# Kernel tuning notes

Hardware: AMD Instinct MI355X
Metric: run time of the kernel (lower is better)

Reference implementation:

```python
import jax, jax.numpy as jnp
import numpy as np

B, S, D = 4, 4096, 1024
THETA = 10000.0


def rope(x):
    # x: [..., S, D]; rotates interleaved (even, odd) dim pairs, standard RoPE.
    s, d = x.shape[-2], x.shape[-1]
    pos = jnp.arange(s, dtype=jnp.float32)
    inv_freq = THETA ** (-jnp.arange(0, d, 2, dtype=jnp.float32) / d)  # [d/2]
    ang = pos[:, None] * inv_freq  # [S, d/2]
    c, sn = jnp.cos(ang), jnp.sin(ang)
    e, o = x[..., ::2], x[..., 1::2]
    re = e * c - o * sn
    ro = e * sn + o * c
    return jnp.stack([re, ro], axis=-1).reshape(x.shape)


def setup_inputs() -> dict:
    key = jax.random.key(0)
    k1, k2, k3, k4 = jax.random.split(key, 4)
    scale = 1.0 / np.sqrt(D)
    return {
        "x": jax.random.normal(k1, (B, S, D), dtype=jnp.float32),
        "Wq": jax.random.normal(k2, (D, D), dtype=jnp.float32) * scale,
        "Wk": jax.random.normal(k3, (D, D), dtype=jnp.float32) * scale,
        "Wv": jax.random.normal(k4, (D, D), dtype=jnp.float32) * scale,
    }


def reference(x, Wq, Wk, Wv):
    # QKV projections (Linear with weight [out, in], no bias)
    Q = rope(x @ Wq.T)
    K = rope(x @ Wk.T)
    V = x @ Wv.T
    d = x.shape[-1]
    s = x.shape[-2]
    scores = jnp.einsum('bqd,bkd->bqk', Q, K) / jnp.sqrt(jnp.asarray(d, Q.dtype))
    causal = jnp.tril(jnp.ones((s, s), dtype=bool))
    scores = jnp.where(causal, scores, -jnp.inf)
    attn = jax.nn.softmax(scores, axis=-1)
    return jnp.einsum('bqk,bkd->bqd', attn, V)
```

## Files before the change

### kernel.cpp

```cpp
#include <hip/hip_runtime.h>
#include <math.h>

#define SQ 4096
#define DM 1024
#define NB 4
#define MT (NB*SQ)
#define XN ((size_t)MT*DM)
#define NCVT 19456
#define NTILES 528
#define STILE 16384

typedef __attribute__((ext_vector_type(4))) float f32x4;
typedef __attribute__((ext_vector_type(8))) short s16x8;

__device__ __forceinline__ unsigned short f2bf(float f) {
  union { float f; unsigned int u; } v; v.f = f;
  unsigned int u = v.u;
  u += 0x7fffu + ((u >> 16) & 1u);
  return (unsigned short)(u >> 16);
}

__device__ __forceinline__ float bf2f(unsigned short u) {
  union { unsigned int i; float f; } v; v.i = ((unsigned int)u) << 16;
  return v.f;
}

__device__ __forceinline__ void async16(const void* g, void* l) {
  __builtin_amdgcn_global_load_lds(
      (const __attribute__((address_space(1))) unsigned int*)g,
      (__attribute__((address_space(3))) unsigned int*)l, 16, 0, 0);
}

__global__ __launch_bounds__(256)
void cvt_all(const float* __restrict__ x, const float* __restrict__ Wq,
             const float* __restrict__ Wk, const float* __restrict__ Wv,
             unsigned short* __restrict__ xb, unsigned short* __restrict__ Wb,
             float* __restrict__ l) {
  if (blockIdx.x >= NCVT) {
    int r = (blockIdx.x - NCVT) * 256 + threadIdx.x;
    l[r] = 0.f;
    return;
  }
  size_t i = ((size_t)blockIdx.x * 256 + threadIdx.x) * 4;
  const float* src; unsigned short* dst;
  if (i < XN) { src = x + i; dst = xb + i; }
  else {
    size_t r = i - XN;
    int w = (int)(r >> 20);
    size_t off = r & (((size_t)1 << 20) - 1);
    src = (w == 0 ? Wq : (w == 1 ? Wk : Wv)) + off;
    dst = Wb + r;
  }
  float4 f = *(const float4*)src;
  ushort4 o;
  o.x = f2bf(f.x); o.y = f2bf(f.y); o.z = f2bf(f.z); o.w = f2bf(f.w);
  *(ushort4*)dst = o;
}

template<int LDA, int LDB>
__device__ __forceinline__ void gemm_tile_body(
    const unsigned short* __restrict__ A, const unsigned short* __restrict__ B,
    unsigned short* As, unsigned short* Bs,
    int m0, int n0, int kext, f32x4 acc[4][4]) {
  const int tid = threadIdx.x, lane = tid & 63, wid = tid >> 6;
  const int quad = lane >> 4, l15 = lane & 15;
  const int wm = wid & 1, wn = wid >> 1;

  const int rbase = wid * 32 + (lane >> 3);
  const int kg8   = ((lane & 7) ^ (lane >> 3)) * 8;
  const unsigned short* Ab = A + (size_t)(m0 + rbase) * LDA + kg8;
  const unsigned short* Bb = B + (size_t)(n0 + rbase) * LDB + kg8;
  unsigned short* Asl = As + (wid * 256 + lane) * 8;
  unsigned short* Bsl = Bs + (wid * 256 + lane) * 8;
  const int xorq = (quad ^ (l15 & 7)) * 8;
  const int am = (wm * 64 + l15) * 64 + xorq;
  const int bn = (wn * 64 + l15) * 64 + xorq;

  for (int k0 = 0; k0 < kext; k0 += 64) {
#pragma unroll
    for (int c = 0; c < 4; c++) {
      async16(Ab + (size_t)c * 8 * LDA + k0, Asl + c * 512);
      async16(Bb + (size_t)c * 8 * LDB + k0, Bsl + c * 512);
    }
    asm volatile("s_waitcnt vmcnt(0)" ::: "memory");
    __syncthreads();
#pragma unroll
    for (int ks = 0; ks < 2; ks++) {
      const int ax = am ^ (ks * 32), bx = bn ^ (ks * 32);
      s16x8 af[4], bfr[4];
#pragma unroll
      for (int t = 0; t < 4; t++) {
        af[t]  = *(const s16x8*)(As + ax + t * 1024);
        bfr[t] = *(const s16x8*)(Bs + bx + t * 1024);
      }
#pragma unroll
      for (int tm = 0; tm < 4; tm++)
#pragma unroll
        for (int tn = 0; tn < 4; tn++)
          acc[tm][tn] = __builtin_amdgcn_mfma_f32_16x16x32_bf16(af[tm], bfr[tn], acc[tm][tn], 0, 0, 0);
    }
    __syncthreads();
  }
}

__global__ __launch_bounds__(256, 3)
void proj_all(const unsigned short* __restrict__ A,
              const unsigned short* __restrict__ Wb,
              unsigned short* __restrict__ QKV) {
  __shared__ unsigned short As[128 * 64];
  __shared__ unsigned short Bs[128 * 64];
  const int lane = threadIdx.x & 63, wid = threadIdx.x >> 6;
  const int quad = lane >> 4, l15 = lane & 15;
  const int wm = wid & 1, wn = wid >> 1;
  const int mat = blockIdx.y >> 3;
  const int m0 = blockIdx.x * 128, n0 = (blockIdx.y & 7) * 128;

  f32x4 zero = {0.f, 0.f, 0.f, 0.f};
  f32x4 acc[4][4];
#pragma unroll
  for (int i = 0; i < 4; i++)
#pragma unroll
    for (int j = 0; j < 4; j++) acc[i][j] = zero;

  gemm_tile_body<DM, DM>(A, Wb + (size_t)mat * DM * DM, As, Bs, m0, n0, DM, acc);

  if (mat < 2) {
    unsigned short* C = QKV + (size_t)mat * XN;
    const bool ev = (lane & 1) == 0;
#pragma unroll
    for (int tm = 0; tm < 4; tm++) {
      int rowb = m0 + wm * 64 + tm * 16 + quad * 4;
#pragma unroll
      for (int tn = 0; tn < 4; tn++) {
        int col = n0 + wn * 64 + tn * 16 + l15;
        f32x4 v = acc[tm][tn];
        float invr = exp2f(-(float)(col & ~1) * (13.287712379549449f / 1024.0f)) * 0.15915494309f;
#pragma unroll
        for (int g = 0; g < 4; g++) {
          int row = rowb + g;
          float rev = (float)(row & (SQ - 1)) * invr;
          rev -= floorf(rev);
          float sn, cs;
          __sincosf(rev * 6.283185307179586f, &sn, &cs);
          float part = __shfl_xor(v[g], 1);
          float e = ev ? v[g] : part;
          float o = ev ? part : v[g];
          float re = e * cs - o * sn;
          float ro = e * sn + o * cs;
          if (ev) {
            unsigned int pk = (unsigned int)f2bf(re) | ((unsigned int)f2bf(ro) << 16);
            *(unsigned int*)(C + (size_t)row * DM + col) = pk;
          }
        }
      }
    }
  } else {
    unsigned short* Vt = QKV + (size_t)2 * XN;
#pragma unroll
    for (int tm = 0; tm < 4; tm++) {
      int rowb = m0 + wm * 64 + tm * 16 + quad * 4;
      int b = rowb >> 12;
      int s = rowb & (SQ - 1);
#pragma unroll
      for (int tn = 0; tn < 4; tn++) {
        int col = n0 + wn * 64 + tn * 16 + l15;
        f32x4 v = acc[tm][tn];
        ushort4 o;
        o.x = f2bf(v[0]); o.y = f2bf(v[1]); o.z = f2bf(v[2]); o.w = f2bf(v[3]);
        *(ushort4*)(Vt + (size_t)b * DM * SQ + (size_t)col * SQ + s) = o;
      }
    }
  }
}

__global__ __launch_bounds__(256, 3)
void qk_gemm(const unsigned short* __restrict__ Q, const unsigned short* __restrict__ K,
             unsigned short* __restrict__ S, float* __restrict__ l) {
  __shared__ unsigned short As[128 * 64];
  __shared__ unsigned short Bs[128 * 64];
  const int lane = threadIdx.x & 63, wid = threadIdx.x >> 6;
  const int quad = lane >> 4, l15 = lane & 15;
  const int wm = wid & 1, wn = wid >> 1;

  const int b = blockIdx.x / NTILES;
  const int t = blockIdx.x - b * NTILES;
  int mt = (int)((sqrtf(8.f * (float)t + 1.f) - 1.f) * 0.5f);
  while ((mt + 1) * (mt + 2) / 2 <= t) ++mt;
  while (mt * (mt + 1) / 2 > t) --mt;
  int nt = t - mt * (mt + 1) / 2;

  const unsigned short* Qg = Q + (size_t)b * SQ * DM;
  const unsigned short* Kg = K + (size_t)b * SQ * DM;
  unsigned short* Sg = S + (size_t)b * NTILES * STILE + ((size_t)t << 14);
  float* lrow = l + b * SQ;

  f32x4 zero = {0.f, 0.f, 0.f, 0.f};
  f32x4 acc[4][4];
#pragma unroll
  for (int i = 0; i < 4; i++)
#pragma unroll
    for (int j = 0; j < 4; j++) acc[i][j] = zero;

  gemm_tile_body<DM, DM>(Qg, Kg, As, Bs, mt * 128, nt * 128, DM, acc);

  const bool ev = (lane & 1) == 0;
#pragma unroll
  for (int tm = 0; tm < 4; tm++) {
    int lr = wm * 64 + tm * 16 + quad * 4;
    int grow = mt * 128 + lr;
    float rsum[4] = {0.f, 0.f, 0.f, 0.f};
#pragma unroll
    for (int tn = 0; tn < 4; tn++) {
      int lc = wn * 64 + tn * 16 + l15;
      int gcol = nt * 128 + lc;
      f32x4 v = acc[tm][tn];
#pragma unroll
      for (int g = 0; g < 4; g++) {
        float p = (gcol <= grow + g) ? __expf(v[g] * 0.03125f) : 0.f;
        rsum[g] += p;
        float part = __shfl_xor(p, 1);
        if (ev) {
          unsigned int pk = (unsigned int)f2bf(p) | ((unsigned int)f2bf(part) << 16);
          *(unsigned int*)(Sg + (size_t)(lr + g) * 128 + lc) = pk;
        }
      }
    }
#pragma unroll
    for (int g = 0; g < 4; g++) {
      float s = rsum[g];
#pragma unroll
      for (int o = 8; o >= 1; o >>= 1) s += __shfl_xor(s, o);
      if (l15 == 0) atomicAdd(&lrow[grow + g], s);
    }
  }
}

__global__ __launch_bounds__(256, 2)
void pv_wide(const unsigned short* __restrict__ P, const unsigned short* __restrict__ Vt,
             const float* __restrict__ l, float* __restrict__ O) {
  __shared__ unsigned short As[128 * 64];
  __shared__ unsigned short Bs[256 * 64];
  const int lane = threadIdx.x & 63, wid = threadIdx.x >> 6;
  const int quad = lane >> 4, l15 = lane & 15;
  const int wm = wid & 1, wn = wid >> 1;
  const int q = blockIdx.x >> 4;
  const int sub = blockIdx.x & 15;
  const int nt = sub >> 2, b = sub & 3;
  const int mt = (q < 16) ? (31 - q) : (q - 16);

  const unsigned short* Pg = P + (size_t)b * NTILES * STILE;
  const unsigned short* Vg = Vt + (size_t)b * DM * SQ;
  const float* lg = l + b * SQ;
  float* Og = O + (size_t)b * SQ * DM;
  const int tribase = mt * (mt + 1) / 2;
  const int n0 = nt * 256;

  const int rbase  = wid * 32 + (lane >> 3);
  const int rbaseB = wid * 64 + (lane >> 3);
  const int kg8 = ((lane & 7) ^ (lane >> 3)) * 8;
  const unsigned short* Bb = Vg + (size_t)(n0 + rbaseB) * SQ + kg8;
  unsigned short* Asl = As + (wid * 256 + lane) * 8;
  unsigned short* Bsl = Bs + (wid * 512 + lane) * 8;
  const int xorq = (quad ^ (l15 & 7)) * 8;
  const int am = (wm * 64 + l15) * 64 + xorq;
  const int bn = (wn * 128 + l15) * 64 + xorq;

  f32x4 zero = {0.f, 0.f, 0.f, 0.f};
  f32x4 acc[4][8];
#pragma unroll
  for (int i = 0; i < 4; i++)
#pragma unroll
    for (int j = 0; j < 8; j++) acc[i][j] = zero;

  const int kext = (mt + 1) * 128;
  for (int k0 = 0; k0 < kext; k0 += 64) {
    const unsigned short* At = Pg + (((size_t)(tribase + (k0 >> 7))) << 14) + (k0 & 64) + kg8;
#pragma unroll
    for (int c = 0; c < 4; c++)
      async16(At + (size_t)(rbase + 8 * c) * 128, Asl + c * 512);
#pragma unroll
    for (int c = 0; c < 8; c++)
      async16(Bb + (size_t)c * 8 * SQ + k0, Bsl + c * 512);
    asm volatile("s_waitcnt vmcnt(0)" ::: "memory");
    __syncthreads();
#pragma unroll
    for (int ks = 0; ks < 2; ks++) {
      const int ax = am ^ (ks * 32), bx2 = bn ^ (ks * 32);
      s16x8 af[4], bfr[8];
#pragma unroll
      for (int t = 0; t < 4; t++) af[t] = *(const s16x8*)(As + ax + t * 1024);
#pragma unroll
      for (int t = 0; t < 8; t++) bfr[t] = *(const s16x8*)(Bs + bx2 + t * 1024);
#pragma unroll
      for (int tm = 0; tm < 4; tm++)
#pragma unroll
        for (int tn = 0; tn < 8; tn++)
          acc[tm][tn] = __builtin_amdgcn_mfma_f32_16x16x32_bf16(af[tm], bfr[tn], acc[tm][tn], 0, 0, 0);
    }
    __syncthreads();
  }

  const bool ev = (lane & 1) == 0;
#pragma unroll
  for (int tm = 0; tm < 4; tm++) {
    int grow = mt * 128 + wm * 64 + tm * 16 + quad * 4;
    float rl[4];
#pragma unroll
    for (int g = 0; g < 4; g++) rl[g] = 1.0f / lg[grow + g];
#pragma unroll
    for (int tn = 0; tn < 8; tn++) {
      int col = n0 + wn * 128 + tn * 16 + l15;
      f32x4 v = acc[tm][tn];
#pragma unroll
      for (int g = 0; g < 4; g++) {
        float val = v[g] * rl[g];
        float part = __shfl_xor(val, 1);
        if (ev) {
          float2 st; st.x = val; st.y = part;
          *(float2*)(Og + (size_t)(grow + g) * DM + col) = st;
        }
      }
    }
  }
}

extern "C" void kernel_launch(void* const* d_in, const int* in_sizes, int n_in,
                              void* d_out, int out_size, void* d_ws, size_t ws_size,
                              hipStream_t stream) {
  const float* x  = (const float*)d_in[0];
  const float* Wq = (const float*)d_in[1];
  const float* Wk = (const float*)d_in[2];
  const float* Wv = (const float*)d_in[3];
  float* out = (float*)d_out;

  unsigned short* Qb  = (unsigned short*)d_ws;
  unsigned short* xb  = Qb + 3 * XN;
  unsigned short* Wb  = xb + XN;
  unsigned short* Sb  = xb;
  float* lfull = (float*)(Sb + (size_t)NB * NTILES * STILE);

  (void)ws_size; (void)in_sizes; (void)n_in; (void)out_size;

  cvt_all<<<NCVT + 64, 256, 0, stream>>>(x, Wq, Wk, Wv, xb, Wb, lfull);

  proj_all<<<dim3(MT / 128, 24), 256, 0, stream>>>(xb, Wb, Qb);

  qk_gemm<<<NB * NTILES, 256, 0, stream>>>(Qb, Qb + XN, Sb, lfull);

  pv_wide<<<512, 256, 0, stream>>>(Sb, Qb + 2 * XN, lfull, out);
}
```

Measured before the change: 451.4 us.

## Enlarge QK and PV attention tiles to 256x256 with 512-thread blocks

Result: slower. 529.0 us (+17.2%).

```diff
diff --git a/kernel.cpp b/kernel.cpp
--- a/kernel.cpp
+++ b/kernel.cpp
@@ -9,6 +9,7 @@
 #define NCVT 19456
 #define NTILES 528
 #define STILE 16384
+#define NT256 136
 
 typedef __attribute__((ext_vector_type(4))) float f32x4;
 typedef __attribute__((ext_vector_type(8))) short s16x8;
@@ -173,17 +174,17 @@
   }
 }
 
-__global__ __launch_bounds__(256, 3)
-void qk_gemm(const unsigned short* __restrict__ Q, const unsigned short* __restrict__ K,
-             unsigned short* __restrict__ S, float* __restrict__ l) {
-  __shared__ unsigned short As[128 * 64];
-  __shared__ unsigned short Bs[128 * 64];
-  const int lane = threadIdx.x & 63, wid = threadIdx.x >> 6;
+__global__ __launch_bounds__(512, 2)
+void qk256(const unsigned short* __restrict__ Q, const unsigned short* __restrict__ K,
+           unsigned short* __restrict__ S, float* __restrict__ l) {
+  __shared__ unsigned short As[256 * 64];
+  __shared__ unsigned short Bs[256 * 64];
+  const int tid = threadIdx.x, lane = tid & 63, wid = tid >> 6;
   const int quad = lane >> 4, l15 = lane & 15;
-  const int wm = wid & 1, wn = wid >> 1;
-
-  const int b = blockIdx.x / NTILES;
-  const int t = blockIdx.x - b * NTILES;
+  const int wm = wid >> 2, wn = wid & 3;
+
+  const int b = blockIdx.x / NT256;
+  int t = blockIdx.x - b * NT256;
   int mt = (int)((sqrtf(8.f * (float)t + 1.f) - 1.f) * 0.5f);
   while ((mt + 1) * (mt + 2) / 2 <= t) ++mt;
   while (mt * (mt + 1) / 2 > t) --mt;
@@ -191,37 +192,77 @@
 
   const unsigned short* Qg = Q + (size_t)b * SQ * DM;
   const unsigned short* Kg = K + (size_t)b * SQ * DM;
-  unsigned short* Sg = S + (size_t)b * NTILES * STILE + ((size_t)t << 14);
+  unsigned short* Sg = S + (size_t)b * NTILES * STILE;
   float* lrow = l + b * SQ;
 
+  const int rstage = wid * 16 + (lane >> 3);
+  const int kg8 = ((lane & 7) ^ (lane >> 3)) * 8;
+  const unsigned short* Ab = Qg + (size_t)(mt * 256 + rstage) * DM + kg8;
+  const unsigned short* Bb = Kg + (size_t)(nt * 256 + rstage) * DM + kg8;
+  unsigned short* Asl = As + wid * 1024 + lane * 8;
+  unsigned short* Bsl = Bs + wid * 1024 + lane * 8;
+  const int xorq = (quad ^ (l15 & 7)) * 8;
+  const int am = (wm * 128 + l15) * 64 + xorq;
+  const int bn = (wn * 64 + l15) * 64 + xorq;
+
   f32x4 zero = {0.f, 0.f, 0.f, 0.f};
-  f32x4 acc[4][4];
-#pragma unroll
-  for (int i = 0; i < 4; i++)
+  f32x4 acc[8][4];
+#pragma unroll
+  for (int i = 0; i < 8; i++)
 #pragma unroll
     for (int j = 0; j < 4; j++) acc[i][j] = zero;
 
-  gemm_tile_body<DM, DM>(Qg, Kg, As, Bs, mt * 128, nt * 128, DM, acc);
+  for (int k0 = 0; k0 < DM; k0 += 64) {
+    async16(Ab + k0, Asl);
+    async16(Ab + (size_t)8 * DM + k0, Asl + 512);
+    async16(Ab + (size_t)128 * DM + k0, Asl + 8192);
+    async16(Ab + (size_t)136 * DM + k0, Asl + 8704);
+    async16(Bb + k0, Bsl);
+    async16(Bb + (size_t)8 * DM + k0, Bsl + 512);
+    async16(Bb + (size_t)128 * DM + k0, Bsl + 8192);
+    async16(Bb + (size_t)136 * DM + k0, Bsl + 8704);
+    asm volatile("s_waitcnt vmcnt(0)" ::: "memory");
+    __syncthreads();
+#pragma unroll
+    for (int ks = 0; ks < 2; ks++) {
+      const int ax = am ^ (ks * 32), bx = bn ^ (ks * 32);
+      s16x8 af[8], bfr[4];
+#pragma unroll
+      for (int u = 0; u < 8; u++) af[u] = *(const s16x8*)(As + ax + u * 1024);
+#pragma unroll
+      for (int u = 0; u < 4; u++) bfr[u] = *(const s16x8*)(Bs + bx + u * 1024);
+#pragma unroll
+      for (int tm = 0; tm < 8; tm++)
+#pragma unroll
+        for (int tn = 0; tn < 4; tn++)
+          acc[tm][tn] = __builtin_amdgcn_mfma_f32_16x16x32_bf16(af[tm], bfr[tn], acc[tm][tn], 0, 0, 0);
+    }
+    __syncthreads();
+  }
 
   const bool ev = (lane & 1) == 0;
 #pragma unroll
-  for (int tm = 0; tm < 4; tm++) {
-    int lr = wm * 64 + tm * 16 + quad * 4;
-    int grow = mt * 128 + lr;
+  for (int tm = 0; tm < 8; tm++) {
+    int lr = wm * 128 + tm * 16 + quad * 4;
+    int grow = mt * 256 + lr;
+    int r128 = mt * 2 + (lr >> 7);
     float rsum[4] = {0.f, 0.f, 0.f, 0.f};
 #pragma unroll
     for (int tn = 0; tn < 4; tn++) {
       int lc = wn * 64 + tn * 16 + l15;
-      int gcol = nt * 128 + lc;
+      int gcol = nt * 256 + lc;
+      int c128 = nt * 2 + (lc >> 7);
+      const bool store = (c128 <= r128);
+      unsigned short* St = Sg + ((size_t)(r128 * (r128 + 1) / 2 + c128) << 14);
       f32x4 v = acc[tm][tn];
 #pragma unroll
       for (int g = 0; g < 4; g++) {
         float p = (gcol <= grow + g) ? __expf(v[g] * 0.03125f) : 0.f;
         rsum[g] += p;
         float part = __shfl_xor(p, 1);
-        if (ev) {
+        if (ev && store) {
           unsigned int pk = (unsigned int)f2bf(p) | ((unsigned int)f2bf(part) << 16);
-          *(unsigned int*)(Sg + (size_t)(lr + g) * 128 + lc) = pk;
+          *(unsigned int*)(St + (size_t)((lr & 127) + g) * 128 + (lc & 127)) = pk;
         }
       }
     }
@@ -235,81 +276,94 @@
   }
 }
 
-__global__ __launch_bounds__(256, 2)
-void pv_wide(const unsigned short* __restrict__ P, const unsigned short* __restrict__ Vt,
-             const float* __restrict__ l, float* __restrict__ O) {
-  __shared__ unsigned short As[128 * 64];
+__global__ __launch_bounds__(512, 2)
+void pv256(const unsigned short* __restrict__ P, const unsigned short* __restrict__ Vt,
+           const float* __restrict__ l, float* __restrict__ O) {
+  __shared__ unsigned short As[256 * 64];
   __shared__ unsigned short Bs[256 * 64];
-  const int lane = threadIdx.x & 63, wid = threadIdx.x >> 6;
+  const int tid = threadIdx.x, lane = tid & 63, wid = tid >> 6;
   const int quad = lane >> 4, l15 = lane & 15;
-  const int wm = wid & 1, wn = wid >> 1;
+  const int wm = wid >> 2, wn = wid & 3;
+
   const int q = blockIdx.x >> 4;
   const int sub = blockIdx.x & 15;
   const int nt = sub >> 2, b = sub & 3;
-  const int mt = (q < 16) ? (31 - q) : (q - 16);
+  const int mt = 15 - q;
 
   const unsigned short* Pg = P + (size_t)b * NTILES * STILE;
   const unsigned short* Vg = Vt + (size_t)b * DM * SQ;
   const float* lg = l + b * SQ;
   float* Og = O + (size_t)b * SQ * DM;
-  const int tribase = mt * (mt + 1) / 2;
+  const int tb0 = (2 * mt) * (2 * mt + 1) / 2;
+  const int tb1 = (2 * mt + 1) * (2 * mt + 2) / 2;
   const int n0 = nt * 256;
 
-  const int rbase  = wid * 32 + (lane >> 3);
-  const int rbaseB = wid * 64 + (lane >> 3);
+  const int rstage = wid * 16 + (lane >> 3);
   const int kg8 = ((lane & 7) ^ (lane >> 3)) * 8;
-  const unsigned short* Bb = Vg + (size_t)(n0 + rbaseB) * SQ + kg8;
-  unsigned short* Asl = As + (wid * 256 + lane) * 8;
-  unsigned short* Bsl = Bs + (wid * 512 + lane) * 8;
+  const unsigned short* Bb = Vg + (size_t)(n0 + rstage) * SQ + kg8;
+  unsigned short* Asl = As + wid * 1024 + lane * 8;
+  unsigned short* Bsl = Bs + wid * 1024 + lane * 8;
   const int xorq = (quad ^ (l15 & 7)) * 8;
-  const int am = (wm * 64 + l15) * 64 + xorq;
-  const int bn = (wn * 128 + l15) * 64 + xorq;
+  const int am = (wm * 128 + l15) * 64 + xorq;
+  const int bn = (wn * 64 + l15) * 64 + xorq;
 
   f32x4 zero = {0.f, 0.f, 0.f, 0.f};
-  f32x4 acc[4][8];
-#pragma unroll
-  for (int i = 0; i < 4; i++)
-#pragma unroll
-    for (int j = 0; j < 8; j++) acc[i][j] = zero;
-
-  const int kext = (mt + 1) * 128;
-  for (int k0 = 0; k0 < kext; k0 += 64) {
-    const unsigned short* At = Pg + (((size_t)(tribase + (k0 >> 7))) << 14) + (k0 & 64) + kg8;
-#pragma unroll
-    for (int c = 0; c < 4; c++)
-      async16(At + (size_t)(rbase + 8 * c) * 128, Asl + c * 512);
-#pragma unroll
-    for (int c = 0; c < 8; c++)
-      async16(Bb + (size_t)c * 8 * SQ + k0, Bsl + c * 512);
-    asm volatile("s_waitcnt vmcnt(0)" ::: "memory");
-    __syncthreads();
-#pragma unroll
-    for (int ks = 0; ks < 2; ks++) {
-      const int ax = am ^ (ks * 32), bx2 = bn ^ (ks * 32);
-      s16x8 af[4], bfr[8];
-#pragma unroll
-      for (int t = 0; t < 4; t++) af[t] = *(const s16x8*)(As + ax + t * 1024);
-#pragma unroll
-      for (int t = 0; t < 8; t++) bfr[t] = *(const s16x8*)(Bs + bx2 + t * 1024);
-#pragma unroll
-      for (int tm = 0; tm < 4; tm++)
-#pragma unroll
-        for (int tn = 0; tn < 8; tn++)
-          acc[tm][tn] = __builtin_amdgcn_mfma_f32_16x16x32_bf16(af[tm], bfr[tn], acc[tm][tn], 0, 0, 0);
-    }
-    __syncthreads();
+  f32x4 acc[8][4];
+#pragma unroll
+  for (int i = 0; i < 8; i++)
+#pragma unroll
+    for (int j = 0; j < 4; j++) acc[i][j] = zero;
+
+  const int jmax = 2 * mt + 1;
+  for (int j = 0; j <= jmax; ++j) {
+    const unsigned short* At0 = Pg + ((size_t)(tb0 + j) << 14) + kg8;
+    const unsigned short* At1 = Pg + ((size_t)(tb1 + j) << 14) + kg8;
+#pragma unroll 1
+    for (int ks2 = 0; ks2 < 2; ks2++) {
+      const int ko = ks2 * 64;
+      if (j < jmax) {
+        async16(At0 + (size_t)rstage * 128 + ko, Asl);
+        async16(At0 + (size_t)(rstage + 8) * 128 + ko, Asl + 512);
+      }
+      async16(At1 + (size_t)rstage * 128 + ko, Asl + 8192);
+      async16(At1 + (size_t)(rstage + 8) * 128 + ko, Asl + 8704);
+      const int k0 = j * 128 + ko;
+      async16(Bb + k0, Bsl);
+      async16(Bb + (size_t)8 * SQ + k0, Bsl + 512);
+      async16(Bb + (size_t)128 * SQ + k0, Bsl + 8192);
+      async16(Bb + (size_t)136 * SQ + k0, Bsl + 8704);
+      asm volatile("s_waitcnt vmcnt(0)" ::: "memory");
+      __syncthreads();
+      if (j < jmax || wm == 1) {
+#pragma unroll
+        for (int ks = 0; ks < 2; ks++) {
+          const int ax = am ^ (ks * 32), bx = bn ^ (ks * 32);
+          s16x8 af[8], bfr[4];
+#pragma unroll
+          for (int u = 0; u < 8; u++) af[u] = *(const s16x8*)(As + ax + u * 1024);
+#pragma unroll
+          for (int u = 0; u < 4; u++) bfr[u] = *(const s16x8*)(Bs + bx + u * 1024);
+#pragma unroll
+          for (int tm = 0; tm < 8; tm++)
+#pragma unroll
+            for (int tn = 0; tn < 4; tn++)
+              acc[tm][tn] = __builtin_amdgcn_mfma_f32_16x16x32_bf16(af[tm], bfr[tn], acc[tm][tn], 0, 0, 0);
+        }
+      }
+      __syncthreads();
+    }
   }
 
   const bool ev = (lane & 1) == 0;
 #pragma unroll
-  for (int tm = 0; tm < 4; tm++) {
-    int grow = mt * 128 + wm * 64 + tm * 16 + quad * 4;
+  for (int tm = 0; tm < 8; tm++) {
+    int grow = mt * 256 + wm * 128 + tm * 16 + quad * 4;
     float rl[4];
 #pragma unroll
     for (int g = 0; g < 4; g++) rl[g] = 1.0f / lg[grow + g];
 #pragma unroll
-    for (int tn = 0; tn < 8; tn++) {
-      int col = n0 + wn * 128 + tn * 16 + l15;
+    for (int tn = 0; tn < 4; tn++) {
+      int col = n0 + wn * 64 + tn * 16 + l15;
       f32x4 v = acc[tm][tn];
 #pragma unroll
       for (int g = 0; g < 4; g++) {
@@ -345,7 +399,7 @@
 
   proj_all<<<dim3(MT / 128, 24), 256, 0, stream>>>(xb, Wb, Qb);
 
-  qk_gemm<<<NB * NTILES, 256, 0, stream>>>(Qb, Qb + XN, Sb, lfull);
-
-  pv_wide<<<512, 256, 0, stream>>>(Sb, Qb + 2 * XN, lfull, out);
-}
+  qk256<<<NB * NT256, 512, 0, stream>>>(Qb, Qb + XN, Sb, lfull);
+
+  pv256<<<256, 512, 0, stream>>>(Sb, Qb + 2 * XN, lfull, out);
+}
```

## Pair causal row tiles per block in PV and remap blocks across XCDs

Applied to the files above, without the earlier changes.

Result: faster. 417.4 us (-7.5%).

```diff
diff --git a/kernel.cpp b/kernel.cpp
--- a/kernel.cpp
+++ b/kernel.cpp
@@ -182,8 +182,9 @@
   const int quad = lane >> 4, l15 = lane & 15;
   const int wm = wid & 1, wn = wid >> 1;
 
-  const int b = blockIdx.x / NTILES;
-  const int t = blockIdx.x - b * NTILES;
+  const int logical = (blockIdx.x & 7) * 264 + (blockIdx.x >> 3);
+  const int b = logical / NTILES;
+  int t = logical - b * NTILES;
   int mt = (int)((sqrtf(8.f * (float)t + 1.f) - 1.f) * 0.5f);
   while ((mt + 1) * (mt + 2) / 2 <= t) ++mt;
   while (mt * (mt + 1) / 2 > t) --mt;
@@ -235,89 +236,97 @@
   }
 }
 
-__global__ __launch_bounds__(256, 2)
-void pv_wide(const unsigned short* __restrict__ P, const unsigned short* __restrict__ Vt,
+__global__ __launch_bounds__(256, 3)
+void pv_pair(const unsigned short* __restrict__ P, const unsigned short* __restrict__ Vt,
              const float* __restrict__ l, float* __restrict__ O) {
   __shared__ unsigned short As[128 * 64];
-  __shared__ unsigned short Bs[256 * 64];
+  __shared__ unsigned short Bs[128 * 64];
   const int lane = threadIdx.x & 63, wid = threadIdx.x >> 6;
   const int quad = lane >> 4, l15 = lane & 15;
   const int wm = wid & 1, wn = wid >> 1;
-  const int q = blockIdx.x >> 4;
-  const int sub = blockIdx.x & 15;
-  const int nt = sub >> 2, b = sub & 3;
-  const int mt = (q < 16) ? (31 - q) : (q - 16);
+
+  const int logical = (blockIdx.x & 7) * 64 + (blockIdx.x >> 3);
+  const int b = logical >> 7;
+  const int p = (logical >> 3) & 15;
+  const int nt = logical & 7;
 
   const unsigned short* Pg = P + (size_t)b * NTILES * STILE;
   const unsigned short* Vg = Vt + (size_t)b * DM * SQ;
   const float* lg = l + b * SQ;
   float* Og = O + (size_t)b * SQ * DM;
-  const int tribase = mt * (mt + 1) / 2;
-  const int n0 = nt * 256;
-
-  const int rbase  = wid * 32 + (lane >> 3);
-  const int rbaseB = wid * 64 + (lane >> 3);
+  const int n0 = nt * 128;
+
+  const int rbase = wid * 32 + (lane >> 3);
   const int kg8 = ((lane & 7) ^ (lane >> 3)) * 8;
-  const unsigned short* Bb = Vg + (size_t)(n0 + rbaseB) * SQ + kg8;
+  const unsigned short* Bb = Vg + (size_t)(n0 + rbase) * SQ + kg8;
   unsigned short* Asl = As + (wid * 256 + lane) * 8;
-  unsigned short* Bsl = Bs + (wid * 512 + lane) * 8;
+  unsigned short* Bsl = Bs + (wid * 256 + lane) * 8;
   const int xorq = (quad ^ (l15 & 7)) * 8;
   const int am = (wm * 64 + l15) * 64 + xorq;
-  const int bn = (wn * 128 + l15) * 64 + xorq;
+  const int bn = (wn * 64 + l15) * 64 + xorq;
+  const bool ev = (lane & 1) == 0;
 
   f32x4 zero = {0.f, 0.f, 0.f, 0.f};
-  f32x4 acc[4][8];
-#pragma unroll
-  for (int i = 0; i < 4; i++)
-#pragma unroll
-    for (int j = 0; j < 8; j++) acc[i][j] = zero;
-
-  const int kext = (mt + 1) * 128;
-  for (int k0 = 0; k0 < kext; k0 += 64) {
-    const unsigned short* At = Pg + (((size_t)(tribase + (k0 >> 7))) << 14) + (k0 & 64) + kg8;
-#pragma unroll
-    for (int c = 0; c < 4; c++)
-      async16(At + (size_t)(rbase + 8 * c) * 128, Asl + c * 512);
-#pragma unroll
-    for (int c = 0; c < 8; c++)
-      async16(Bb + (size_t)c * 8 * SQ + k0, Bsl + c * 512);
-    asm volatile("s_waitcnt vmcnt(0)" ::: "memory");
-    __syncthreads();
-#pragma unroll
-    for (int ks = 0; ks < 2; ks++) {
-      const int ax = am ^ (ks * 32), bx2 = bn ^ (ks * 32);
-      s16x8 af[4], bfr[8];
-#pragma unroll
-      for (int t = 0; t < 4; t++) af[t] = *(const s16x8*)(As + ax + t * 1024);
-#pragma unroll
-      for (int t = 0; t < 8; t++) bfr[t] = *(const s16x8*)(Bs + bx2 + t * 1024);
-#pragma unroll
-      for (int tm = 0; tm < 4; tm++)
-#pragma unroll
-        for (int tn = 0; tn < 8; tn++)
-          acc[tm][tn] = __builtin_amdgcn_mfma_f32_16x16x32_bf16(af[tm], bfr[tn], acc[tm][tn], 0, 0, 0);
-    }
-    __syncthreads();
-  }
-
-  const bool ev = (lane & 1) == 0;
-#pragma unroll
-  for (int tm = 0; tm < 4; tm++) {
-    int grow = mt * 128 + wm * 64 + tm * 16 + quad * 4;
-    float rl[4];
-#pragma unroll
-    for (int g = 0; g < 4; g++) rl[g] = 1.0f / lg[grow + g];
-#pragma unroll
-    for (int tn = 0; tn < 8; tn++) {
-      int col = n0 + wn * 128 + tn * 16 + l15;
-      f32x4 v = acc[tm][tn];
-#pragma unroll
-      for (int g = 0; g < 4; g++) {
-        float val = v[g] * rl[g];
-        float part = __shfl_xor(val, 1);
-        if (ev) {
-          float2 st; st.x = val; st.y = part;
-          *(float2*)(Og + (size_t)(grow + g) * DM + col) = st;
+#pragma unroll 1
+  for (int half = 0; half < 2; half++) {
+    const int mt = half ? (31 - p) : p;
+    const int tb = mt * (mt + 1) / 2;
+    f32x4 acc[4][4];
+#pragma unroll
+    for (int i = 0; i < 4; i++)
+#pragma unroll
+      for (int j = 0; j < 4; j++) acc[i][j] = zero;
+
+    for (int j = 0; j <= mt; ++j) {
+      const unsigned short* At = Pg + ((size_t)(tb + j) << 14) + kg8;
+      const int kbase = j * 128;
+#pragma unroll 1
+      for (int ks2 = 0; ks2 < 2; ks2++) {
+        const int ko = ks2 * 64;
+#pragma unroll
+        for (int c = 0; c < 4; c++) {
+          async16(At + (size_t)(rbase + 8 * c) * 128 + ko, Asl + c * 512);
+          async16(Bb + (size_t)c * 8 * SQ + kbase + ko, Bsl + c * 512);
+        }
+        asm volatile("s_waitcnt vmcnt(0)" ::: "memory");
+        __syncthreads();
+#pragma unroll
+        for (int ks = 0; ks < 2; ks++) {
+          const int ax = am ^ (ks * 32), bx = bn ^ (ks * 32);
+          s16x8 af[4], bfr[4];
+#pragma unroll
+          for (int u = 0; u < 4; u++) {
+            af[u]  = *(const s16x8*)(As + ax + u * 1024);
+            bfr[u] = *(const s16x8*)(Bs + bx + u * 1024);
+          }
+#pragma unroll
+          for (int tm = 0; tm < 4; tm++)
+#pragma unroll
+            for (int tn = 0; tn < 4; tn++)
+              acc[tm][tn] = __builtin_amdgcn_mfma_f32_16x16x32_bf16(af[tm], bfr[tn], acc[tm][tn], 0, 0, 0);
+        }
+        __syncthreads();
+      }
+    }
+
+#pragma unroll
+    for (int tm = 0; tm < 4; tm++) {
+      int grow = mt * 128 + wm * 64 + tm * 16 + quad * 4;
+      float rl[4];
+#pragma unroll
+      for (int g = 0; g < 4; g++) rl[g] = 1.0f / lg[grow + g];
+#pragma unroll
+      for (int tn = 0; tn < 4; tn++) {
+        int col = n0 + wn * 64 + tn * 16 + l15;
+        f32x4 v = acc[tm][tn];
+#pragma unroll
+        for (int g = 0; g < 4; g++) {
+          float val = v[g] * rl[g];
+          float part = __shfl_xor(val, 1);
+          if (ev) {
+            float2 st; st.x = val; st.y = part;
+            *(float2*)(Og + (size_t)(grow + g) * DM + col) = st;
+          }
         }
       }
     }
@@ -347,5 +356,5 @@
 
   qk_gemm<<<NB * NTILES, 256, 0, stream>>>(Qb, Qb + XN, Sb, lfull);
 
-  pv_wide<<<512, 256, 0, stream>>>(Sb, Qb + 2 * XN, lfull, out);
-}
+  pv_pair<<<512, 256, 0, stream>>>(Sb, Qb + 2 * XN, lfull, out);
+}
```
